# Optimization experiments

Hardware: AMD Instinct MI355X
Metric: run time of the kernel (lower is better)

## Reference

```python
import jax, jax.numpy as jnp
import numpy as np

EMB_DIMS = 1024

def setup_inputs() -> dict:
    key = jax.random.key(0)
    k1, k2, k3 = jax.random.split(key, 3)
    B, S, D = 4, 2048, EMB_DIMS
    x = jax.random.normal(k1, (B, S, D), dtype=jnp.float32)
    # nn.Linear(D, 3D): weight stored as [3D, D] in torch; we use [D, 3D] (x @ W)
    w_qkv = jax.random.normal(k2, (D, 3 * D), dtype=jnp.float32) * (D ** -0.5)
    b_qkv = jax.random.normal(k3, (3 * D,), dtype=jnp.float32) * 0.01
    return {"x": x, "w_qkv": w_qkv, "b_qkv": b_qkv}

def reference(x, w_qkv, b_qkv):
    D = x.shape[-1]
    scale = D ** (-0.5)  # torch code divides qk by this (i.e. multiplies by sqrt(D))
    qkv = x @ w_qkv + b_qkv                      # [B,S,3D]
    q, k, v = jnp.split(qkv, 3, axis=-1)         # each [B,S,D]
    scores = jnp.einsum('bsd,btd->bst', q, k) / scale  # [B,S,S]
    attn = jax.nn.sigmoid(scores)                # sigmoid, NOT softmax
    return jnp.einsum('bst,btd->bsd', attn, v)   # [B,S,D]
```

## Files before the change

### kernel.cpp

```cpp
#include <hip/hip_runtime.h>
#include <stdint.h>

typedef unsigned short u16;
typedef _Float16 f16x8 __attribute__((ext_vector_type(8)));
typedef float f32x4 __attribute__((ext_vector_type(4)));

#define B_   4
#define S_   2048
#define D_   1024
#define ND3  3072

__device__ __forceinline__ u16 f2h(float x) {
    union { _Float16 h; u16 u; } v; v.h = (_Float16)x; return v.u;
}

__device__ __forceinline__ void gload_lds16(const u16* g, u16* l) {
    __builtin_amdgcn_global_load_lds((const __attribute__((address_space(1))) void*)g,
                                     (__attribute__((address_space(3))) void*)l, 16, 0, 0);
}

__device__ __forceinline__ int xcd_swz(int lid, int nwg) {
    int c = nwg >> 3;
    return (lid & 7) * c + (lid >> 3);
}

template<int NT>
__device__ __forceinline__ void gemm_wide(const u16* __restrict__ A, const u16* __restrict__ Bt,
                                          int lda, int ldb, int rowbase, int colbase,
                                          u16* ldsA, u16* ldsB, f32x4 (&acc)[4][4])
{
    const int NSTEP = 2 * NT;
    const int tid  = threadIdx.x;
    const int lane = tid & 63;
    const int w    = tid >> 6;
    const int wr   = w >> 2, wc = w & 3;

    const int r0 = tid >> 2;
    const int c0 = (((tid & 3) ^ ((tid >> 3) & 3)) << 3);
    const uint32_t offA0 = (uint32_t)(rowbase + r0) * lda + c0;
    const uint32_t offB0 = (uint32_t)(colbase + r0) * ldb + c0;
    const uint32_t offB1 = offB0 + (uint32_t)128 * ldb;
    const int dst = tid << 3;

    const int rd_lane = ((lane & 15) << 5) + ((((lane >> 4) ^ (lane >> 1)) & 3) << 3);
    const int wrOff = wr << 11;
    const int wcOff = wc << 11;

#define ISSUE(sv) do { int s_ = (sv); \
    if (s_ < NSTEP) { \
        uint32_t ko_ = (uint32_t)s_ << 5; \
        int st_ = s_ % 3; \
        int slA_ = st_ << 12; \
        int slB_ = st_ << 13; \
        gload_lds16(A  + offA0 + ko_, ldsA + slA_ + dst); \
        gload_lds16(Bt + offB0 + ko_, ldsB + slB_ + dst); \
        gload_lds16(Bt + offB1 + ko_, ldsB + slB_ + dst + 4096); \
    } } while (0)

    f16x8 af[4], bf[4];

    ISSUE(0); ISSUE(1);
    int sl = 0;
    for (int S = 0; S < NSTEP; ++S) {
        asm volatile("s_waitcnt lgkmcnt(0)" ::: "memory");
        if (S < NSTEP - 1) asm volatile("s_waitcnt vmcnt(3)" ::: "memory");
        else               asm volatile("s_waitcnt vmcnt(0)" ::: "memory");
        __builtin_amdgcn_s_barrier();
        asm volatile("" ::: "memory");
        ISSUE(S + 2);
        const int slA = sl << 12, slB = sl << 13;
#pragma unroll
        for (int mq = 0; mq < 4; ++mq)
            af[mq] = *(const f16x8*)(ldsA + slA + wrOff + (mq << 9) + rd_lane);
#pragma unroll
        for (int n = 0; n < 4; ++n)
            bf[n] = *(const f16x8*)(ldsB + slB + wcOff + (n << 9) + rd_lane);
#pragma unroll
        for (int mq = 0; mq < 4; ++mq)
#pragma unroll
            for (int n = 0; n < 4; ++n)
                acc[mq][n] = __builtin_amdgcn_mfma_f32_16x16x32_f16(af[mq], bf[n], acc[mq][n], 0, 0, 0);
        sl = (sl == 2) ? 0 : sl + 1;
    }
#undef ISSUE
}

__global__ __launch_bounds__(256) void k_prep(const float* __restrict__ x, u16* __restrict__ xh,
                                              const float* __restrict__ W, u16* __restrict__ Wt) {
    __shared__ float t[32][33];
    int bb = blockIdx.x;
    if (bb < 4096) {
        int i = (bb * 256 + threadIdx.x) << 3;
        if (i >= B_ * S_ * D_) return;
        float4 a = *(const float4*)(x + i);
        float4 b = *(const float4*)(x + i + 4);
        ushort4 h0, h1;
        h0.x = f2h(a.x); h0.y = f2h(a.y); h0.z = f2h(a.z); h0.w = f2h(a.w);
        h1.x = f2h(b.x); h1.y = f2h(b.y); h1.z = f2h(b.z); h1.w = f2h(b.w);
        *(ushort4*)(xh + i)     = h0;
        *(ushort4*)(xh + i + 4) = h1;
    } else {
        bb -= 4096;
        int c0 = (bb % 96) << 5, r0 = (bb / 96) << 5;
        int tx = threadIdx.x & 31, ty = threadIdx.x >> 5;
#pragma unroll
        for (int i = 0; i < 4; ++i) {
            int r = (i << 3) + ty;
            t[r][tx] = W[(size_t)(r0 + r) * ND3 + c0 + tx];
        }
        __syncthreads();
#pragma unroll
        for (int i = 0; i < 4; ++i) {
            int r = (i << 3) + ty;
            Wt[(size_t)(c0 + r) * D_ + r0 + tx] = f2h(t[tx][r]);
        }
    }
}

__global__ __launch_bounds__(512, 4) void k_qkv(const u16* __restrict__ xh,
                                                const u16* __restrict__ wt,
                                                const float* __restrict__ bias,
                                                u16* __restrict__ qf, u16* __restrict__ kf,
                                                u16* __restrict__ vt) {
    __shared__ u16 lds[36864];
    f32x4 acc[4][4];
    f32x4 z = {0.f, 0.f, 0.f, 0.f};
#pragma unroll
    for (int m = 0; m < 4; ++m)
#pragma unroll
        for (int n = 0; n < 4; ++n) acc[m][n] = z;

    const int lid = blockIdx.y * 12 + blockIdx.x;
    const int swz = xcd_swz(lid, 768);
    const int bx = swz % 12, by = swz / 12;
    const int rowbase = by << 7;
    const int colbase = bx << 8;
    gemm_wide<16>(xh, wt, D_, D_, rowbase, colbase, lds, lds + 12288, acc);

    const int lane = threadIdx.x & 63;
    const int w = threadIdx.x >> 6;
    const int wr = w >> 2, wc = w & 3;
    const int region = colbase >> 10;
#pragma unroll
    for (int m = 0; m < 4; ++m) {
        int gr0 = rowbase + wr * 64 + m * 16 + ((lane >> 4) << 2);
#pragma unroll
        for (int n = 0; n < 4; ++n) {
            int gc = colbase + wc * 64 + n * 16 + (lane & 15);
            float bv = bias[gc];
            if (region == 0) {
#pragma unroll
                for (int r = 0; r < 4; ++r)
                    qf[(size_t)(gr0 + r) * D_ + gc] = f2h(acc[m][n][r] + bv);
            } else if (region == 1) {
                int c = gc - 1024;
#pragma unroll
                for (int r = 0; r < 4; ++r)
                    kf[(size_t)(gr0 + r) * D_ + c] = f2h(acc[m][n][r] + bv);
            } else {
                int d  = gc - 2048;
                int b  = gr0 >> 11;
                int t0 = gr0 & 2047;
                size_t base = (((size_t)b << 10) + d) * (size_t)S_ + t0;
#pragma unroll
                for (int r = 0; r < 4; ++r)
                    vt[base + r] = f2h(acc[m][n][r] + bv);
            }
        }
    }
}

__global__ __launch_bounds__(512, 4) void k_scores(const u16* __restrict__ qf,
                                                   const u16* __restrict__ kf,
                                                   u16* __restrict__ attn) {
    __shared__ u16 lds[36864];
    f32x4 acc[4][4];
    f32x4 z = {0.f, 0.f, 0.f, 0.f};
#pragma unroll
    for (int m = 0; m < 4; ++m)
#pragma unroll
        for (int n = 0; n < 4; ++n) acc[m][n] = z;

    const int m_ = (blockIdx.z << 4) + blockIdx.y;
    const int P  = (blockIdx.x << 3) + (m_ >> 3);
    const int bx = m_ & 7, by = P & 15, b = P >> 4;

    const size_t boff = (size_t)b * S_ * D_;
    u16* att = attn + (size_t)b * S_ * S_;
    const int rowbase = by << 7, colbase = bx << 8;
    gemm_wide<16>(qf + boff, kf + boff, D_, D_, rowbase, colbase, lds, lds + 12288, acc);

    const int lane = threadIdx.x & 63;
    const int w = threadIdx.x >> 6;
    const int wr = w >> 2, wc = w & 3;
#pragma unroll
    for (int m = 0; m < 4; ++m) {
        int gr0 = rowbase + wr * 64 + m * 16 + ((lane >> 4) << 2);
#pragma unroll
        for (int n = 0; n < 4; ++n) {
            int gc = colbase + wc * 64 + n * 16 + (lane & 15);
#pragma unroll
            for (int r = 0; r < 4; ++r) {
                float sv = acc[m][n][r] * 32.0f;
                float sg = 1.0f / (1.0f + __expf(-sv));
                att[(size_t)(gr0 + r) * S_ + gc] = f2h(sg);
            }
        }
    }
}

__global__ __launch_bounds__(512, 4) void k_pv(const u16* __restrict__ attn,
                                               const u16* __restrict__ vt,
                                               float* __restrict__ out) {
    __shared__ u16 lds[36864];
    f32x4 acc[4][4];
    f32x4 z = {0.f, 0.f, 0.f, 0.f};
#pragma unroll
    for (int m = 0; m < 4; ++m)
#pragma unroll
        for (int n = 0; n < 4; ++n) acc[m][n] = z;

    const int lid = (blockIdx.z << 6) + (blockIdx.y << 2) + blockIdx.x;
    const int swz = xcd_swz(lid, 256);
    const int bx = swz & 3, by = (swz >> 2) & 15, b = swz >> 6;

    const u16* Aa = attn + (size_t)b * S_ * S_;
    const u16* Bv = vt   + (size_t)b * D_ * S_;
    float* ob     = out  + (size_t)b * S_ * D_;
    const int rowbase = by << 7, colbase = bx << 8;
    gemm_wide<32>(Aa, Bv, S_, S_, rowbase, colbase, lds, lds + 12288, acc);

    const int lane = threadIdx.x & 63;
    const int w = threadIdx.x >> 6;
    const int wr = w >> 2, wc = w & 3;
#pragma unroll
    for (int m = 0; m < 4; ++m) {
        int gr0 = rowbase + wr * 64 + m * 16 + ((lane >> 4) << 2);
#pragma unroll
        for (int n = 0; n < 4; ++n) {
            int gc = colbase + wc * 64 + n * 16 + (lane & 15);
#pragma unroll
            for (int r = 0; r < 4; ++r)
                ob[(size_t)(gr0 + r) * D_ + gc] = acc[m][n][r];
        }
    }
}

extern "C" void kernel_launch(void* const* d_in, const int* in_sizes, int n_in,
                              void* d_out, int out_size, void* d_ws, size_t ws_size,
                              hipStream_t stream) {
    const float* x    = (const float*)d_in[0];
    const float* wqkv = (const float*)d_in[1];
    const float* bias = (const float*)d_in[2];
    float* out = (float*)d_out;

    const size_t MB = 1048576;
    uint8_t* ws = (uint8_t*)d_ws;
    u16* xh   = (u16*)(ws);
    u16* wt   = (u16*)(ws + 16 * MB);
    u16* qf   = (u16*)(ws + 32 * MB);
    u16* kf   = (u16*)(ws + 48 * MB);
    u16* vt   = (u16*)(ws + 64 * MB);
    u16* attn = (u16*)(ws);

    k_prep<<<dim3(4096 + 3072), dim3(256), 0, stream>>>(x, xh, wqkv, wt);
    k_qkv<<<dim3(ND3 / 256, (B_ * S_) / 128), dim3(512), 0, stream>>>(xh, wt, bias, qf, kf, vt);
    k_scores<<<dim3(S_ / 256, S_ / 128, B_), dim3(512), 0, stream>>>(qf, kf, attn);
    k_pv<<<dim3(D_ / 256, S_ / 128, B_), dim3(512), 0, stream>>>(attn, vt, out);
}
```

Before: 156.8 us.

## Use 4 waves per block with 128x64 per-wave tiles in GEMM kernels

Switches the three GEMM kernels from 512-thread blocks with 2x4 waves, each computing 64x64, to 256-thread blocks where each of 4 waves computes 128x64 (8x4 MFMA tiles). The block tile stays 128x256, so each thread now issues twice as many global-to-LDS loads, and the wait counts are adjusted to match. Each wave reuses its B fragments across twice as many A fragments, which raises MFMA work per LDS read. The cost is double the accumulator registers and fewer waves for hiding latency.

Measured after the change: 168.8 us. 7.7% more time.

```diff
diff --git a/kernel.cpp b/kernel.cpp
--- a/kernel.cpp
+++ b/kernel.cpp
@@ -25,58 +25,63 @@
 }
 
 template<int NT>
-__device__ __forceinline__ void gemm_wide(const u16* __restrict__ A, const u16* __restrict__ Bt,
-                                          int lda, int ldb, int rowbase, int colbase,
-                                          u16* ldsA, u16* ldsB, f32x4 (&acc)[4][4])
+__device__ __forceinline__ void gemm_big(const u16* __restrict__ A, const u16* __restrict__ Bt,
+                                         int lda, int ldb, int rowbase, int colbase,
+                                         u16* ldsA, u16* ldsB, f32x4 (&acc)[8][4])
 {
     const int NSTEP = 2 * NT;
     const int tid  = threadIdx.x;
     const int lane = tid & 63;
-    const int w    = tid >> 6;
-    const int wr   = w >> 2, wc = w & 3;
-
-    const int r0 = tid >> 2;
-    const int c0 = (((tid & 3) ^ ((tid >> 3) & 3)) << 3);
-    const uint32_t offA0 = (uint32_t)(rowbase + r0) * lda + c0;
-    const uint32_t offB0 = (uint32_t)(colbase + r0) * ldb + c0;
-    const uint32_t offB1 = offB0 + (uint32_t)128 * ldb;
-    const int dst = tid << 3;
+    const int wc   = (tid >> 6) & 3;
+
+    const int vA0 = tid, vA1 = tid + 256;
+    const uint32_t offA0 = (uint32_t)(rowbase + (vA0 >> 2)) * lda + (((vA0 & 3) ^ ((vA0 >> 3) & 3)) << 3);
+    const uint32_t offA1 = (uint32_t)(rowbase + (vA1 >> 2)) * lda + (((vA1 & 3) ^ ((vA1 >> 3) & 3)) << 3);
+    uint32_t offB[4];
+    int dstB[4];
+#pragma unroll
+    for (int j = 0; j < 4; ++j) {
+        int v = tid + (j << 8);
+        offB[j] = (uint32_t)(colbase + (v >> 2)) * ldb + (((v & 3) ^ ((v >> 3) & 3)) << 3);
+        dstB[j] = v << 3;
+    }
+    const int dstA0 = vA0 << 3, dstA1 = vA1 << 3;
 
     const int rd_lane = ((lane & 15) << 5) + ((((lane >> 4) ^ (lane >> 1)) & 3) << 3);
-    const int wrOff = wr << 11;
     const int wcOff = wc << 11;
 
 #define ISSUE(sv) do { int s_ = (sv); \
     if (s_ < NSTEP) { \
         uint32_t ko_ = (uint32_t)s_ << 5; \
         int st_ = s_ % 3; \
-        int slA_ = st_ << 12; \
-        int slB_ = st_ << 13; \
-        gload_lds16(A  + offA0 + ko_, ldsA + slA_ + dst); \
-        gload_lds16(Bt + offB0 + ko_, ldsB + slB_ + dst); \
-        gload_lds16(Bt + offB1 + ko_, ldsB + slB_ + dst + 4096); \
+        int slA_ = st_ << 12;              \
+        int slB_ = st_ << 13;              \
+        gload_lds16(A + offA0 + ko_, ldsA + slA_ + dstA0); \
+        gload_lds16(A + offA1 + ko_, ldsA + slA_ + dstA1); \
+        _Pragma("unroll") for (int j = 0; j < 4; ++j) \
+            gload_lds16(Bt + offB[j] + ko_, ldsB + slB_ + dstB[j]); \
     } } while (0)
 
-    f16x8 af[4], bf[4];
+    f16x8 af[8], bf[4];
 
     ISSUE(0); ISSUE(1);
     int sl = 0;
     for (int S = 0; S < NSTEP; ++S) {
         asm volatile("s_waitcnt lgkmcnt(0)" ::: "memory");
-        if (S < NSTEP - 1) asm volatile("s_waitcnt vmcnt(3)" ::: "memory");
+        if (S < NSTEP - 1) asm volatile("s_waitcnt vmcnt(6)" ::: "memory");
         else               asm volatile("s_waitcnt vmcnt(0)" ::: "memory");
         __builtin_amdgcn_s_barrier();
         asm volatile("" ::: "memory");
         ISSUE(S + 2);
         const int slA = sl << 12, slB = sl << 13;
 #pragma unroll
-        for (int mq = 0; mq < 4; ++mq)
-            af[mq] = *(const f16x8*)(ldsA + slA + wrOff + (mq << 9) + rd_lane);
+        for (int mq = 0; mq < 8; ++mq)
+            af[mq] = *(const f16x8*)(ldsA + slA + (mq << 9) + rd_lane);
 #pragma unroll
         for (int n = 0; n < 4; ++n)
             bf[n] = *(const f16x8*)(ldsB + slB + wcOff + (n << 9) + rd_lane);
 #pragma unroll
-        for (int mq = 0; mq < 4; ++mq)
+        for (int mq = 0; mq < 8; ++mq)
 #pragma unroll
             for (int n = 0; n < 4; ++n)
                 acc[mq][n] = __builtin_amdgcn_mfma_f32_16x16x32_f16(af[mq], bf[n], acc[mq][n], 0, 0, 0);
@@ -117,16 +122,16 @@
     }
 }
 
-__global__ __launch_bounds__(512, 4) void k_qkv(const u16* __restrict__ xh,
+__global__ __launch_bounds__(256, 2) void k_qkv(const u16* __restrict__ xh,
                                                 const u16* __restrict__ wt,
                                                 const float* __restrict__ bias,
                                                 u16* __restrict__ qf, u16* __restrict__ kf,
                                                 u16* __restrict__ vt) {
     __shared__ u16 lds[36864];
-    f32x4 acc[4][4];
+    f32x4 acc[8][4];
     f32x4 z = {0.f, 0.f, 0.f, 0.f};
 #pragma unroll
-    for (int m = 0; m < 4; ++m)
+    for (int m = 0; m < 8; ++m)
 #pragma unroll
         for (int n = 0; n < 4; ++n) acc[m][n] = z;
 
@@ -135,15 +140,14 @@
     const int bx = swz % 12, by = swz / 12;
     const int rowbase = by << 7;
     const int colbase = bx << 8;
-    gemm_wide<16>(xh, wt, D_, D_, rowbase, colbase, lds, lds + 12288, acc);
+    gemm_big<16>(xh, wt, D_, D_, rowbase, colbase, lds, lds + 12288, acc);
 
     const int lane = threadIdx.x & 63;
-    const int w = threadIdx.x >> 6;
-    const int wr = w >> 2, wc = w & 3;
+    const int wc = (threadIdx.x >> 6) & 3;
     const int region = colbase >> 10;
 #pragma unroll
-    for (int m = 0; m < 4; ++m) {
-        int gr0 = rowbase + wr * 64 + m * 16 + ((lane >> 4) << 2);
+    for (int m = 0; m < 8; ++m) {
+        int gr0 = rowbase + m * 16 + ((lane >> 4) << 2);
 #pragma unroll
         for (int n = 0; n < 4; ++n) {
             int gc = colbase + wc * 64 + n * 16 + (lane & 15);
@@ -170,14 +174,14 @@
     }
 }
 
-__global__ __launch_bounds__(512, 4) void k_scores(const u16* __restrict__ qf,
+__global__ __launch_bounds__(256, 2) void k_scores(const u16* __restrict__ qf,
                                                    const u16* __restrict__ kf,
                                                    u16* __restrict__ attn) {
     __shared__ u16 lds[36864];
-    f32x4 acc[4][4];
+    f32x4 acc[8][4];
     f32x4 z = {0.f, 0.f, 0.f, 0.f};
 #pragma unroll
-    for (int m = 0; m < 4; ++m)
+    for (int m = 0; m < 8; ++m)
 #pragma unroll
         for (int n = 0; n < 4; ++n) acc[m][n] = z;
 
@@ -188,14 +192,13 @@
     const size_t boff = (size_t)b * S_ * D_;
     u16* att = attn + (size_t)b * S_ * S_;
     const int rowbase = by << 7, colbase = bx << 8;
-    gemm_wide<16>(qf + boff, kf + boff, D_, D_, rowbase, colbase, lds, lds + 12288, acc);
+    gemm_big<16>(qf + boff, kf + boff, D_, D_, rowbase, colbase, lds, lds + 12288, acc);
 
     const int lane = threadIdx.x & 63;
-    const int w = threadIdx.x >> 6;
-    const int wr = w >> 2, wc = w & 3;
-#pragma unroll
-    for (int m = 0; m < 4; ++m) {
-        int gr0 = rowbase + wr * 64 + m * 16 + ((lane >> 4) << 2);
+    const int wc = (threadIdx.x >> 6) & 3;
+#pragma unroll
+    for (int m = 0; m < 8; ++m) {
+        int gr0 = rowbase + m * 16 + ((lane >> 4) << 2);
 #pragma unroll
         for (int n = 0; n < 4; ++n) {
             int gc = colbase + wc * 64 + n * 16 + (lane & 15);
@@ -209,14 +212,14 @@
     }
 }
 
-__global__ __launch_bounds__(512, 4) void k_pv(const u16* __restrict__ attn,
+__global__ __launch_bounds__(256, 2) void k_pv(const u16* __restrict__ attn,
                                                const u16* __restrict__ vt,
                                                float* __restrict__ out) {
     __shared__ u16 lds[36864];
-    f32x4 acc[4][4];
+    f32x4 acc[8][4];
     f32x4 z = {0.f, 0.f, 0.f, 0.f};
 #pragma unroll
-    for (int m = 0; m < 4; ++m)
+    for (int m = 0; m < 8; ++m)
 #pragma unroll
         for (int n = 0; n < 4; ++n) acc[m][n] = z;
 
@@ -228,14 +231,13 @@
     const u16* Bv = vt   + (size_t)b * D_ * S_;
     float* ob     = out  + (size_t)b * S_ * D_;
     const int rowbase = by << 7, colbase = bx << 8;
-    gemm_wide<32>(Aa, Bv, S_, S_, rowbase, colbase, lds, lds + 12288, acc);
+    gemm_big<32>(Aa, Bv, S_, S_, rowbase, colbase, lds, lds + 12288, acc);
 
     const int lane = threadIdx.x & 63;
-    const int w = threadIdx.x >> 6;
-    const int wr = w >> 2, wc = w & 3;
-#pragma unroll
-    for (int m = 0; m < 4; ++m) {
-        int gr0 = rowbase + wr * 64 + m * 16 + ((lane >> 4) << 2);
+    const int wc = (threadIdx.x >> 6) & 3;
+#pragma unroll
+    for (int m = 0; m < 8; ++m) {
+        int gr0 = rowbase + m * 16 + ((lane >> 4) << 2);
 #pragma unroll
         for (int n = 0; n < 4; ++n) {
             int gc = colbase + wc * 64 + n * 16 + (lane & 15);
@@ -264,7 +266,7 @@
     u16* attn = (u16*)(ws);
 
     k_prep<<<dim3(4096 + 3072), dim3(256), 0, stream>>>(x, xh, wqkv, wt);
-    k_qkv<<<dim3(ND3 / 256, (B_ * S_) / 128), dim3(512), 0, stream>>>(xh, wt, bias, qf, kf, vt);
-    k_scores<<<dim3(S_ / 256, S_ / 128, B_), dim3(512), 0, stream>>>(qf, kf, attn);
-    k_pv<<<dim3(D_ / 256, S_ / 128, B_), dim3(512), 0, stream>>>(attn, vt, out);
-}
+    k_qkv<<<dim3(ND3 / 256, (B_ * S_) / 128), dim3(256), 0, stream>>>(xh, wt, bias, qf, kf, vt);
+    k_scores<<<dim3(S_ / 256, S_ / 128, B_), dim3(256), 0, stream>>>(qf, kf, attn);
+    k_pv<<<dim3(D_ / 256, S_ / 128, B_), dim3(256), 0, stream>>>(attn, vt, out);
+}
```
